# Optimization experiments

Measured on AMD Instinct MI355X. Metric: run time of the kernel, lower is better.

## Reference

```python
import jax, jax.numpy as jnp
import numpy as np

B = 8          # batch
S = 256        # nx+1 = ny+1 grid resolution
N = S * S      # number of DoFs per component
DIM = 2        # output vector dimension (= d_out)
W = 32         # FNO channel width
M1 = 12        # Fourier modes dim 1
M2 = 12        # Fourier modes dim 2
WF = 128       # final MLP hidden width
NL = 4         # number of Fourier layers
PADF = 8       # padding fraction denominator


def setup_inputs() -> dict:
    key = jax.random.key(0)
    ks = jax.random.split(key, 16)
    sc = 1.0 / (W * W)  # torch FNO spectral weight init scale
    return {
        "x": jax.random.normal(ks[0], (B, N), jnp.float32),
        "d2v_in": jax.random.permutation(ks[1], jnp.arange(N)),
        "v2d_out": jax.random.permutation(ks[2], jnp.arange(N)),
        "fc0_w": jax.random.normal(ks[3], (W, 3), jnp.float32) * 0.1,
        "fc0_b": jnp.zeros((W,), jnp.float32),
        "spec_w1r": jax.random.uniform(ks[4], (NL, W, W, M1, M2), jnp.float32) * sc,
        "spec_w1i": jax.random.uniform(ks[5], (NL, W, W, M1, M2), jnp.float32) * sc,
        "spec_w2r": jax.random.uniform(ks[6], (NL, W, W, M1, M2), jnp.float32) * sc,
        "spec_w2i": jax.random.uniform(ks[7], (NL, W, W, M1, M2), jnp.float32) * sc,
        "conv_w": jax.random.normal(ks[8], (NL, W, W), jnp.float32) * 0.05,
        "conv_b": jnp.zeros((NL, W), jnp.float32),
        "mlp_w1": jax.random.normal(ks[9], (WF, W), jnp.float32) * 0.05,
        "mlp_b1": jnp.zeros((WF,), jnp.float32),
        "mlp_w2": jax.random.normal(ks[10], (DIM, WF), jnp.float32) * 0.05,
        "mlp_b2": jnp.zeros((DIM,), jnp.float32),
    }


def _speconv(x, w1, w2):
    # x: (B, C, H, Wd) real; w1/w2: (C_in, C_out, M1, M2) complex64
    Bh, C, H, Wd = x.shape
    xft = jnp.fft.rfft2(x)  # (B, C, H, Wd//2+1)
    o1 = jnp.einsum('bixy,ioxy->boxy', xft[:, :, :M1, :M2], w1)
    o2 = jnp.einsum('bixy,ioxy->boxy', xft[:, :, -M1:, :M2], w2)
    out_ft = jnp.zeros((Bh, C, H, Wd // 2 + 1), jnp.complex64)
    out_ft = out_ft.at[:, :, :M1, :M2].set(o1).at[:, :, -M1:, :M2].set(o2)
    return jnp.fft.irfft2(out_ft, s=(H, Wd))


def reference(x, d2v_in, v2d_out, fc0_w, fc0_b,
              spec_w1r, spec_w1i, spec_w2r, spec_w2i,
              conv_w, conv_b, mlp_w1, mlp_b1, mlp_w2, mlp_b2):
    # DoF -> vertex gather and lift to image
    xg = x[:, d2v_in].reshape(B, 1, S, S)
    h = jnp.transpose(xg, (0, 2, 3, 1))  # (B, S, S, 1)
    # append normalized grid coordinates (get_grid2d)
    g = jnp.linspace(0.0, 1.0, S, dtype=jnp.float32)
    grid = jnp.stack(jnp.meshgrid(g, g, indexing='ij'), axis=-1)  # (S, S, 2)
    grid = jnp.broadcast_to(grid[None], (B, S, S, 2))
    h = jnp.concatenate([h, grid], axis=-1)
    # fc0 lifting
    h = h @ fc0_w.T + fc0_b              # (B, S, S, W)
    h = jnp.transpose(h, (0, 3, 1, 2))   # (B, W, S, S)
    # zero pad (non-periodic domain)
    p = S // PADF
    h = jnp.pad(h, ((0, 0), (0, 0), (0, p), (0, p)))  # (B, W, S+p, S+p)
    w1 = (spec_w1r + 1j * spec_w1i).astype(jnp.complex64)
    w2 = (spec_w2r + 1j * spec_w2i).astype(jnp.complex64)
    for l in range(NL):
        sp = _speconv(h, w1[l], w2[l])
        cv = jnp.einsum('bchw,oc->bohw', h, conv_w[l]) + conv_b[l][None, :, None, None]
        h = cv + sp
        if l != NL - 1:
            h = jax.nn.gelu(h, approximate=False)  # torch GELU default = exact erf
    # crop padding (s_outputspace=None path)
    h = h[..., :S, :S]
    # final two-layer MLP projection
    h = jnp.transpose(h, (0, 2, 3, 1))  # (B, S, S, W)
    h = jax.nn.gelu(h @ mlp_w1.T + mlp_b1, approximate=False) @ mlp_w2.T + mlp_b2
    h = jnp.transpose(h, (0, 3, 1, 2)).reshape(B, DIM, -1)  # (B, DIM, N)
    # vertex -> DoF scatter/gather and interleave components
    out = h[:, :, v2d_out]              # (B, DIM, N)
    out = jnp.transpose(out, (0, 2, 1)).reshape(B, -1)  # (B, N*DIM)
    return out
```

## Files before the change

### kernel.cpp

```cpp
#include <hip/hip_runtime.h>
#include <math.h>

#define S    256
#define Hp   288
#define C    32
#define KY   12
#define NK   24
#define Bn   8
#define PI_D 3.14159265358979323846264338327950288

#define SZ_TW  (NK*Hp*2)
#define OFF_TW 0
#define OFF_TWT (OFF_TW + SZ_TW)
#define SZ_TWT (Hp*KY*2)
#define OFF_H  (OFF_TWT + SZ_TWT)
#define SZ_H   (Bn*C*Hp*Hp)
#define OFF_Y  (OFF_H + SZ_H)
#define SZ_Y   (Bn*C*Hp*KY*2)
#define OFF_X  (OFF_Y + SZ_Y)
#define SZ_X   (Bn*C*NK*KY*2)
#define OFF_Z  (OFF_X + 2*SZ_X)
#define SZ_Z   (Bn*Hp*C*KY*2)
#define OFF_T  (OFF_Z + SZ_Z)
#define SZ_T   (Bn*S*S*2)

#define GELU(v) (0.5f*(v)*(1.0f+erff((v)*0.70710678118654752f)))
#define SCHED_FENCE() __builtin_amdgcn_sched_barrier(0)

#if __has_builtin(__builtin_amdgcn_global_load_lds)
#define HAS_ASYNC 1
#define ASYNC_CP16(dst, src) \
    __builtin_amdgcn_global_load_lds((const __attribute__((address_space(1))) void*)(src), \
                                     (__attribute__((address_space(3))) void*)(dst), 16, 0, 0)
#else
#define HAS_ASYNC 0
#endif

__global__ void k_tw(float* __restrict__ tw, float* __restrict__ twT) {
    int i = blockIdx.x * 256 + threadIdx.x;
    if (i >= NK * Hp) return;
    int k = i / Hp, xx = i % Hp;
    int f = (k < KY) ? k : (k + 264);
    int m = (f * xx) % Hp;
    double th = (2.0 * PI_D * (double)m) / (double)Hp;
    float c = (float)cos(th), s = (float)sin(th);
    tw[2 * i] = c; tw[2 * i + 1] = s;
    if (k < KY) { twT[xx * 24 + 2 * k] = c; twT[xx * 24 + 2 * k + 1] = s; }
}

template<int Q>
__device__ __forceinline__ void embed_body(
        const float* __restrict__ xs, const float* __restrict__ twq,
        float* __restrict__ h, size_t rowbase, int o, int g,
        float w0, float w1, float w2, float bb, float gx,
        float* pr, float* pi) {
    #pragma unroll 1
    for (int c3 = 0; c3 < 3; ++c3) {
        int ybase = g * 36 + c3 * 12;
        int rowq  = (g & 1) * 36 + c3 * 12;
        float acc[12];
        #pragma unroll
        for (int j = 0; j < 12; ++j) {
            int y = ybase + j;
            acc[j] = (y < S) ? (w0 * xs[y < S ? y : 0] + w1 * gx + w2 * (y * (1.0f / 255.0f)) + bb) : 0.f;
        }
        float* hw = h + rowbase + (size_t)o * 82944 + ybase;
        #pragma unroll
        for (int q = 0; q < 3; ++q)
            *(float4*)&hw[4 * q] = make_float4(acc[4*q], acc[4*q+1], acc[4*q+2], acc[4*q+3]);
        SCHED_FENCE();
        #pragma unroll
        for (int jp = 0; jp < 6; ++jp) {
            #pragma unroll
            for (int u = 0; u < 2; ++u) {
                int j = jp * 2 + u;
                const float* tg = twq + (rowq + j) * 24;
                float tc[24];
                #pragma unroll
                for (int q = 0; q < 6; ++q) *(float4*)&tc[4 * q] = *(const float4*)&tg[4 * q];
                float v = acc[j];
                pr[0] += v;
                #pragma unroll
                for (int k = 1; k < 12; ++k) {
                    const int e = (k * Q) & 3;
                    float c = tc[2 * k], s = tc[2 * k + 1];
                    if      (e == 0) { pr[k] += v * c; pi[k] -= v * s; }
                    else if (e == 1) { pr[k] -= v * s; pi[k] -= v * c; }
                    else if (e == 2) { pr[k] -= v * c; pi[k] += v * s; }
                    else             { pr[k] += v * s; pi[k] += v * c; }
                }
            }
            SCHED_FENCE();
        }
    }
}

__global__ __launch_bounds__(256, 1) void k_embed(
        const float* __restrict__ xin, const int* __restrict__ d2v,
        const float* __restrict__ fw, const float* __restrict__ fb,
        const float* __restrict__ twT, float* __restrict__ h, float* __restrict__ Y) {
    __shared__ __align__(16) float xs[256];
    __shared__ __align__(16) float twq[1728];
    __shared__ __align__(16) float YP[3072];
    int x = blockIdx.x, b = blockIdx.y, tid = threadIdx.x;
    size_t rowbase = (size_t)b * 2654208 + (size_t)x * 288;
    if (x >= S) {
        for (int i = tid; i < 32 * 72; i += 256) {
            int c = i / 72, q = i % 72;
            *(float4*)&h[rowbase + (size_t)c * 82944 + q * 4] = make_float4(0, 0, 0, 0);
        }
        for (int i = tid; i < 768; i += 256)
            Y[((size_t)(b * 32 + i / 24) * 288 + x) * 24 + (i % 24)] = 0.f;
        return;
    }
    for (int i = tid; i < 432; i += 256)
        *(float4*)&twq[4 * i] = *(const float4*)&twT[4 * i];
    xs[tid] = xin[b * 65536 + d2v[x * 256 + tid]];
    int o = tid & 31, g = tid >> 5;
    float w0 = fw[o * 3], w1 = fw[o * 3 + 1], w2 = fw[o * 3 + 2], bb = fb[o];
    float gx = x * (1.0f / 255.0f);
    __syncthreads();
    float pr[12], pi[12];
    #pragma unroll
    for (int k = 0; k < 12; ++k) { pr[k] = 0.f; pi[k] = 0.f; }
    switch (tid >> 6) {
        case 0: embed_body<0>(xs, twq, h, rowbase, o, g, w0, w1, w2, bb, gx, pr, pi); break;
        case 1: embed_body<1>(xs, twq, h, rowbase, o, g, w0, w1, w2, bb, gx, pr, pi); break;
        case 2: embed_body<2>(xs, twq, h, rowbase, o, g, w0, w1, w2, bb, gx, pr, pi); break;
        default: embed_body<3>(xs, twq, h, rowbase, o, g, w0, w1, w2, bb, gx, pr, pi); break;
    }
    #pragma unroll
    for (int k = 0; k < 12; ++k) { pr[k] += __shfl_xor(pr[k], 32); pi[k] += __shfl_xor(pi[k], 32); }
    if ((tid & 32) == 0) {
        float* dst = YP + ((tid >> 6) * 32 + o) * 24;
        #pragma unroll
        for (int k = 0; k < 12; ++k) { dst[2 * k] = pr[k]; dst[2 * k + 1] = pi[k]; }
    }
    __syncthreads();
    for (int i = tid; i < 768; i += 256) {
        float s = YP[i] + YP[768 + i] + YP[1536 + i] + YP[2304 + i];
        Y[((size_t)(b * 32 + i / 24) * 288 + x) * 24 + (i % 24)] = s;
    }
}

__global__ __launch_bounds__(288) void k_dftx(const float* __restrict__ Y,
                                              const float* __restrict__ tw,
                                              float* __restrict__ X) {
    __shared__ __align__(16) float Ys[144 * 24];
    int c = blockIdx.x, b = blockIdx.y, half = blockIdx.z, tid = threadIdx.x;
    const float* Yb = Y + (size_t)(b * 32 + c) * 6912 + half * 3456;
    for (int i = tid; i < 864; i += 288)
        *(float4*)&Ys[4 * i] = *(const float4*)&Yb[4 * i];
    __syncthreads();
    int k = tid / 12, ky = tid % 12;
    const float* twk = tw + k * 576 + half * 288;
    float xr = 0.f, xi = 0.f;
    #pragma unroll 4
    for (int xx = 0; xx < 144; ++xx) {
        float yr = Ys[xx * 24 + 2 * ky], yi = Ys[xx * 24 + 2 * ky + 1];
        float cc = twk[2 * xx], ss = twk[2 * xx + 1];
        xr += yr * cc + yi * ss;
        xi += yi * cc - yr * ss;
    }
    size_t oo = (size_t)half * SZ_X + ((size_t)(b * 32 + c) * 288 + tid) * 2;
    X[oo] = xr; X[oo + 1] = xi;
}

__global__ __launch_bounds__(384) void k_specidft(
        const float* __restrict__ X,
        const float* __restrict__ w1r, const float* __restrict__ w1i,
        const float* __restrict__ w2r, const float* __restrict__ w2i,
        const float* __restrict__ tw, float* __restrict__ Z, int l) {
    __shared__ __align__(16) float Os[576];
    int x0 = blockIdx.x * 32, c = blockIdx.y, b = blockIdx.z, tid = threadIdx.x;
    if (tid < 288) {
        int k = tid / 12, ky = tid % 12;
        int kk = (k < KY) ? k : (k - KY);
        const float* wr = (k < KY) ? w1r : w2r;
        const float* wi = (k < KY) ? w1i : w2i;
        size_t wbase = (size_t)l * 147456 + (size_t)c * 144 + kk * 12 + ky;
        size_t xbase = (size_t)b * 18432 + (k * 12 + ky) * 2;
        float ar = 0.f, ai = 0.f;
        #pragma unroll 8
        for (int i = 0; i < 32; ++i) {
            size_t xo = xbase + (size_t)i * 576;
            float xr = X[xo]     + X[SZ_X + xo];
            float xi = X[xo + 1] + X[SZ_X + xo + 1];
            float wrr = wr[wbase + (size_t)i * 4608];
            float wii = wi[wbase + (size_t)i * 4608];
            ar += xr * wrr - xi * wii;
            ai += xr * wii + xi * wrr;
        }
        Os[2 * tid] = ar; Os[2 * tid + 1] = ai;
    }
    __syncthreads();
    int row = tid & 31, ky = tid >> 5;
    int x = x0 + row;
    float zr = 0.f, zi = 0.f;
    #pragma unroll
    for (int k = 0; k < NK; ++k) {
        float orr = Os[(k * 12 + ky) * 2], oii = Os[(k * 12 + ky) * 2 + 1];
        float cc = tw[(k * Hp + x) * 2], ss = tw[(k * Hp + x) * 2 + 1];
        zr += orr * cc - oii * ss;
        zi += orr * ss + oii * cc;
    }
    size_t o = ((((size_t)b * Hp + x) * C + c) * KY + ky) * 2;
    Z[o] = zr; Z[o + 1] = zi;
}

__global__ __launch_bounds__(256, 1) void k_conv(
        float* __restrict__ h, const float* __restrict__ Z,
        const float* __restrict__ cw, const float* __restrict__ cb,
        const float* __restrict__ twT, float* __restrict__ Y,
        int l, int flags) {
    __shared__ __align__(16) float hs[9216];
    __shared__ __align__(16) float twy[6912];
    __shared__ __align__(16) float cws[32 * 33];
    __shared__ float cbs[32];
    int x = blockIdx.x, b = blockIdx.y, tid = threadIdx.x;
    size_t rowbase = (size_t)b * 2654208 + (size_t)x * 288;
    const float* hb = h + rowbase;
#if HAS_ASYNC
    #pragma unroll 1
    for (int r = 0; r < 9; ++r) {
        int i = r * 256 + tid;
        ASYNC_CP16(&hs[4 * i], hb + (size_t)(i / 72) * 82944 + (i % 72) * 4);
    }
    #pragma unroll 1
    for (int i = tid; i < 1728; i += 256)
        ASYNC_CP16(&twy[4 * i], twT + 4 * i);
#else
    for (int i = tid; i < 2304; i += 256)
        *(float4*)&hs[4 * i] = *(const float4*)&hb[(size_t)(i / 72) * 82944 + (i % 72) * 4];
    for (int i = tid; i < 1728; i += 256)
        *(float4*)&twy[4 * i] = *(const float4*)&twT[4 * i];
#endif
    for (int i = tid; i < 32 * 32; i += 256)
        cws[(i >> 5) * 33 + (i & 31)] = cw[l * 1024 + i];
    if (tid < 32) cbs[tid] = cb[l * 32 + tid];
    int o = tid & 31, g = tid >> 5;
    const float* Zr = Z + ((size_t)(b * 288 + x) * 32 + o) * 24;
    float zr[12], zi[12];
    #pragma unroll
    for (int q = 0; q < 6; ++q) {
        float4 zv = *(const float4*)&Zr[4 * q];
        zr[2*q] = zv.x; zi[2*q] = zv.y; zr[2*q+1] = zv.z; zi[2*q+1] = zv.w;
    }
    __syncthreads();
    float bias = cbs[o];
    float pr[12], pi[12];
    #pragma unroll
    for (int k = 0; k < 12; ++k) { pr[k] = 0.f; pi[k] = 0.f; }
    const int gelu_f = flags & 1, wy = flags & 2;
    #pragma unroll 1
    for (int c3 = 0; c3 < 3; ++c3) {
        int ybase = g * 36 + c3 * 12;
        float acc[12];
        #pragma unroll
        for (int j = 0; j < 12; ++j) acc[j] = bias;
        #pragma unroll 8
        for (int c = 0; c < 32; ++c) {
            float w = cws[o * 33 + c];
            const float* hr = &hs[c * 288 + ybase];
            float4 h0 = *(const float4*)&hr[0];
            float4 h1 = *(const float4*)&hr[4];
            float4 h2 = *(const float4*)&hr[8];
            acc[0] += h0.x * w; acc[1] += h0.y * w; acc[2]  += h0.z * w; acc[3]  += h0.w * w;
            acc[4] += h1.x * w; acc[5] += h1.y * w; acc[6]  += h1.z * w; acc[7]  += h1.w * w;
            acc[8] += h2.x * w; acc[9] += h2.y * w; acc[10] += h2.z * w; acc[11] += h2.w * w;
        }
        SCHED_FENCE();
        #pragma unroll
        for (int jp = 0; jp < 6; ++jp) {
            #pragma unroll
            for (int u = 0; u < 2; ++u) {
                int j = jp * 2 + u;
                int y = ybase + j;
                float tc[24];
                #pragma unroll
                for (int q = 0; q < 6; ++q) *(float4*)&tc[4 * q] = *(const float4*)&twy[y * 24 + 4 * q];
                float sp = zr[0] * tc[0] - zi[0] * tc[1];
                #pragma unroll
                for (int k = 1; k < 12; ++k) sp += 2.f * (zr[k] * tc[2*k] - zi[k] * tc[2*k+1]);
                float val = acc[j] + sp * (1.0f / 82944.0f);
                if (gelu_f) val = GELU(val);
                acc[j] = val;
                if (wy) {
                    #pragma unroll
                    for (int k = 0; k < 12; ++k) { pr[k] += val * tc[2*k]; pi[k] -= val * tc[2*k+1]; }
                }
            }
            SCHED_FENCE();
        }
        float* hw = h + rowbase + (size_t)o * 82944 + ybase;
        #pragma unroll
        for (int q = 0; q < 3; ++q)
            *(float4*)&hw[4 * q] = make_float4(acc[4*q], acc[4*q+1], acc[4*q+2], acc[4*q+3]);
        SCHED_FENCE();
    }
    if (wy) {
        #pragma unroll
        for (int k = 0; k < 12; ++k) { pr[k] += __shfl_xor(pr[k], 32); pi[k] += __shfl_xor(pi[k], 32); }
        __syncthreads();
        float* YP = hs;
        if ((tid & 32) == 0) {
            float* dst = YP + ((tid >> 6) * 32 + o) * 24;
            #pragma unroll
            for (int k = 0; k < 12; ++k) { dst[2 * k] = pr[k]; dst[2 * k + 1] = pi[k]; }
        }
        __syncthreads();
        for (int i = tid; i < 768; i += 256) {
            float s = YP[i] + YP[768 + i] + YP[1536 + i] + YP[2304 + i];
            Y[((size_t)(b * 32 + i / 24) * 288 + x) * 24 + (i % 24)] = s;
        }
    }
}

__global__ __launch_bounds__(256) void k_mlp(const float* __restrict__ h,
                                             const float* __restrict__ w1, const float* __restrict__ b1,
                                             const float* __restrict__ w2, const float* __restrict__ b2,
                                             float* __restrict__ tmp) {
    int bid = blockIdx.x;
    int b = bid >> 7;
    int x = ((bid & 127) << 1) + (threadIdx.x >> 7);
    int lane = threadIdx.x & 127;
    const float* hb = h + (size_t)b * 2654208 + (size_t)x * 288;
    float hc0[32], hc1[32];
    #pragma unroll
    for (int c = 0; c < 32; ++c) {
        hc0[c] = hb[(size_t)c * 82944 + lane];
        hc1[c] = hb[(size_t)c * 82944 + lane + 128];
    }
    float o00 = 0.f, o01 = 0.f, o10 = 0.f, o11 = 0.f;
    for (int f = 0; f < 128; ++f) {
        float a0 = b1[f], a1 = a0;
        #pragma unroll
        for (int c = 0; c < 32; ++c) {
            float w = w1[f * 32 + c];
            a0 += hc0[c] * w; a1 += hc1[c] * w;
        }
        float wa = w2[f], wb = w2[128 + f];
        float g0 = GELU(a0), g1 = GELU(a1);
        o00 += g0 * wa; o01 += g0 * wb;
        o10 += g1 * wa; o11 += g1 * wb;
    }
    float bb0 = b2[0], bb1 = b2[1];
    int p0 = x * 256 + lane;
    size_t base = (size_t)b * 65536;
    *(float2*)&tmp[(base + p0) * 2]       = make_float2(o00 + bb0, o01 + bb1);
    *(float2*)&tmp[(base + p0 + 128) * 2] = make_float2(o10 + bb0, o11 + bb1);
}

__global__ void k_scatter(const float* __restrict__ tmp, const int* __restrict__ v2d,
                          float* __restrict__ out) {
    int id = blockIdx.x * 256 + threadIdx.x;
    int b = id >> 16; int j = id & 65535;
    int p = v2d[j];
    const float2 v = *(const float2*)(tmp + ((size_t)(b << 16) + p) * 2);
    *(float2*)(out + (size_t)id * 2) = v;
}

extern "C" void kernel_launch(void* const* d_in, const int* in_sizes, int n_in,
                              void* d_out, int out_size, void* d_ws, size_t ws_size,
                              hipStream_t stream) {
    const float* xin   = (const float*)d_in[0];
    const int*   d2v   = (const int*)  d_in[1];
    const int*   v2d   = (const int*)  d_in[2];
    const float* fc0w  = (const float*)d_in[3];
    const float* fc0b  = (const float*)d_in[4];
    const float* w1r   = (const float*)d_in[5];
    const float* w1i   = (const float*)d_in[6];
    const float* w2r   = (const float*)d_in[7];
    const float* w2i   = (const float*)d_in[8];
    const float* cw    = (const float*)d_in[9];
    const float* cb    = (const float*)d_in[10];
    const float* mw1   = (const float*)d_in[11];
    const float* mb1   = (const float*)d_in[12];
    const float* mw2   = (const float*)d_in[13];
    const float* mb2   = (const float*)d_in[14];

    float* ws  = (float*)d_ws;
    float* TW  = ws + OFF_TW;
    float* TWT = ws + OFF_TWT;
    float* H   = ws + OFF_H;
    float* Y   = ws + OFF_Y;
    float* X   = ws + OFF_X;
    float* Z   = ws + OFF_Z;
    float* T   = ws + OFF_T;

    k_tw<<<(NK * Hp + 255) / 256, 256, 0, stream>>>(TW, TWT);
    k_embed<<<dim3(Hp, Bn), 256, 0, stream>>>(xin, d2v, fc0w, fc0b, TWT, H, Y);

    for (int l = 0; l < 4; ++l) {
        k_dftx<<<dim3(32, Bn, 2), 288, 0, stream>>>(Y, TW, X);
        k_specidft<<<dim3(9, 32, Bn), 384, 0, stream>>>(X, w1r, w1i, w2r, w2i, TW, Z, l);
        k_conv<<<dim3((l != 3) ? Hp : S, Bn), 256, 0, stream>>>(H, Z, cw, cb, TWT, Y, l, (l != 3) ? 3 : 0);
    }

    k_mlp<<<1024, 256, 0, stream>>>(H, mw1, mb1, mw2, mb2, T);
    k_scatter<<<(Bn * S * S) / 256, 256, 0, stream>>>(T, v2d, (float*)d_out);
}
```

Measured before the change: 812.8 us.

## Fuse last Fourier layer conv with final MLP projection into one kernel

Measured after the change: 1.046 ms. 28.7% more time.

```diff
diff --git a/kernel.cpp b/kernel.cpp
--- a/kernel.cpp
+++ b/kernel.cpp
@@ -208,11 +208,45 @@
     Z[o] = zr; Z[o + 1] = zi;
 }
 
+__device__ __forceinline__ void conv12(const float* __restrict__ hs,
+                                       const float* __restrict__ cws,
+                                       int o, int ybase, float bias, float* acc) {
+    #pragma unroll
+    for (int j = 0; j < 12; ++j) acc[j] = bias;
+    #pragma unroll 8
+    for (int c = 0; c < 32; ++c) {
+        float w = cws[o * 33 + c];
+        const float* hr = &hs[c * 288 + ybase];
+        float4 h0 = *(const float4*)&hr[0];
+        float4 h1 = *(const float4*)&hr[4];
+        float4 h2 = *(const float4*)&hr[8];
+        acc[0] += h0.x * w; acc[1] += h0.y * w; acc[2]  += h0.z * w; acc[3]  += h0.w * w;
+        acc[4] += h1.x * w; acc[5] += h1.y * w; acc[6]  += h1.z * w; acc[7]  += h1.w * w;
+        acc[8] += h2.x * w; acc[9] += h2.y * w; acc[10] += h2.z * w; acc[11] += h2.w * w;
+    }
+    SCHED_FENCE();
+}
+
+__device__ __forceinline__ void epi12_plain(const float* __restrict__ twy, int ybase,
+                                            float* acc, const float* zr, const float* zi) {
+    #pragma unroll
+    for (int j = 0; j < 12; ++j) {
+        const float* tg = twy + (ybase + j) * 24;
+        float tc[24];
+        #pragma unroll
+        for (int q = 0; q < 6; ++q) *(float4*)&tc[4 * q] = *(const float4*)&tg[4 * q];
+        float sp = zr[0] * tc[0] - zi[0] * tc[1];
+        #pragma unroll
+        for (int k = 1; k < 12; ++k) sp += 2.f * (zr[k] * tc[2*k] - zi[k] * tc[2*k+1]);
+        acc[j] += sp * (1.0f / 82944.0f);
+        if (j & 1) SCHED_FENCE();
+    }
+}
+
 __global__ __launch_bounds__(256, 1) void k_conv(
         float* __restrict__ h, const float* __restrict__ Z,
         const float* __restrict__ cw, const float* __restrict__ cb,
-        const float* __restrict__ twT, float* __restrict__ Y,
-        int l, int flags) {
+        const float* __restrict__ twT, float* __restrict__ Y, int l) {
     __shared__ __align__(16) float hs[9216];
     __shared__ __align__(16) float twy[6912];
     __shared__ __align__(16) float cws[32 * 33];
@@ -251,25 +285,11 @@
     float pr[12], pi[12];
     #pragma unroll
     for (int k = 0; k < 12; ++k) { pr[k] = 0.f; pi[k] = 0.f; }
-    const int gelu_f = flags & 1, wy = flags & 2;
     #pragma unroll 1
     for (int c3 = 0; c3 < 3; ++c3) {
         int ybase = g * 36 + c3 * 12;
         float acc[12];
-        #pragma unroll
-        for (int j = 0; j < 12; ++j) acc[j] = bias;
-        #pragma unroll 8
-        for (int c = 0; c < 32; ++c) {
-            float w = cws[o * 33 + c];
-            const float* hr = &hs[c * 288 + ybase];
-            float4 h0 = *(const float4*)&hr[0];
-            float4 h1 = *(const float4*)&hr[4];
-            float4 h2 = *(const float4*)&hr[8];
-            acc[0] += h0.x * w; acc[1] += h0.y * w; acc[2]  += h0.z * w; acc[3]  += h0.w * w;
-            acc[4] += h1.x * w; acc[5] += h1.y * w; acc[6]  += h1.z * w; acc[7]  += h1.w * w;
-            acc[8] += h2.x * w; acc[9] += h2.y * w; acc[10] += h2.z * w; acc[11] += h2.w * w;
-        }
-        SCHED_FENCE();
+        conv12(hs, cws, o, ybase, bias, acc);
         #pragma unroll
         for (int jp = 0; jp < 6; ++jp) {
             #pragma unroll
@@ -283,12 +303,10 @@
                 #pragma unroll
                 for (int k = 1; k < 12; ++k) sp += 2.f * (zr[k] * tc[2*k] - zi[k] * tc[2*k+1]);
                 float val = acc[j] + sp * (1.0f / 82944.0f);
-                if (gelu_f) val = GELU(val);
+                val = GELU(val);
                 acc[j] = val;
-                if (wy) {
-                    #pragma unroll
-                    for (int k = 0; k < 12; ++k) { pr[k] += val * tc[2*k]; pi[k] -= val * tc[2*k+1]; }
-                }
+                #pragma unroll
+                for (int k = 0; k < 12; ++k) { pr[k] += val * tc[2*k]; pi[k] -= val * tc[2*k+1]; }
             }
             SCHED_FENCE();
         }
@@ -298,57 +316,96 @@
             *(float4*)&hw[4 * q] = make_float4(acc[4*q], acc[4*q+1], acc[4*q+2], acc[4*q+3]);
         SCHED_FENCE();
     }
-    if (wy) {
-        #pragma unroll
-        for (int k = 0; k < 12; ++k) { pr[k] += __shfl_xor(pr[k], 32); pi[k] += __shfl_xor(pi[k], 32); }
-        __syncthreads();
-        float* YP = hs;
-        if ((tid & 32) == 0) {
-            float* dst = YP + ((tid >> 6) * 32 + o) * 24;
-            #pragma unroll
-            for (int k = 0; k < 12; ++k) { dst[2 * k] = pr[k]; dst[2 * k + 1] = pi[k]; }
-        }
-        __syncthreads();
-        for (int i = tid; i < 768; i += 256) {
-            float s = YP[i] + YP[768 + i] + YP[1536 + i] + YP[2304 + i];
-            Y[((size_t)(b * 32 + i / 24) * 288 + x) * 24 + (i % 24)] = s;
-        }
-    }
-}
-
-__global__ __launch_bounds__(256) void k_mlp(const float* __restrict__ h,
-                                             const float* __restrict__ w1, const float* __restrict__ b1,
-                                             const float* __restrict__ w2, const float* __restrict__ b2,
-                                             float* __restrict__ tmp) {
-    int bid = blockIdx.x;
-    int b = bid >> 7;
-    int x = ((bid & 127) << 1) + (threadIdx.x >> 7);
-    int lane = threadIdx.x & 127;
-    const float* hb = h + (size_t)b * 2654208 + (size_t)x * 288;
-    float hc0[32], hc1[32];
-    #pragma unroll
-    for (int c = 0; c < 32; ++c) {
-        hc0[c] = hb[(size_t)c * 82944 + lane];
-        hc1[c] = hb[(size_t)c * 82944 + lane + 128];
-    }
-    float o00 = 0.f, o01 = 0.f, o10 = 0.f, o11 = 0.f;
+    #pragma unroll
+    for (int k = 0; k < 12; ++k) { pr[k] += __shfl_xor(pr[k], 32); pi[k] += __shfl_xor(pi[k], 32); }
+    __syncthreads();
+    float* YP = hs;
+    if ((tid & 32) == 0) {
+        float* dst = YP + ((tid >> 6) * 32 + o) * 24;
+        #pragma unroll
+        for (int k = 0; k < 12; ++k) { dst[2 * k] = pr[k]; dst[2 * k + 1] = pi[k]; }
+    }
+    __syncthreads();
+    for (int i = tid; i < 768; i += 256) {
+        float s = YP[i] + YP[768 + i] + YP[1536 + i] + YP[2304 + i];
+        Y[((size_t)(b * 32 + i / 24) * 288 + x) * 24 + (i % 24)] = s;
+    }
+}
+
+__global__ __launch_bounds__(256, 1) void k_convmlp(
+        const float* __restrict__ h, const float* __restrict__ Z,
+        const float* __restrict__ cw, const float* __restrict__ cb,
+        const float* __restrict__ twT,
+        const float* __restrict__ mw1, const float* __restrict__ mb1,
+        const float* __restrict__ mw2, const float* __restrict__ mb2,
+        float* __restrict__ tmp) {
+    __shared__ __align__(16) float hs[9216];
+    __shared__ __align__(16) float twy[6912];
+    __shared__ __align__(16) float cws[32 * 33];
+    __shared__ float cbs[32];
+    int x = blockIdx.x, b = blockIdx.y, tid = threadIdx.x;
+    size_t rowbase = (size_t)b * 2654208 + (size_t)x * 288;
+    const float* hb = h + rowbase;
+#if HAS_ASYNC
+    #pragma unroll 1
+    for (int r = 0; r < 9; ++r) {
+        int i = r * 256 + tid;
+        ASYNC_CP16(&hs[4 * i], hb + (size_t)(i / 72) * 82944 + (i % 72) * 4);
+    }
+    #pragma unroll 1
+    for (int i = tid; i < 1728; i += 256)
+        ASYNC_CP16(&twy[4 * i], twT + 4 * i);
+#else
+    for (int i = tid; i < 2304; i += 256)
+        *(float4*)&hs[4 * i] = *(const float4*)&hb[(size_t)(i / 72) * 82944 + (i % 72) * 4];
+    for (int i = tid; i < 1728; i += 256)
+        *(float4*)&twy[4 * i] = *(const float4*)&twT[4 * i];
+#endif
+    for (int i = tid; i < 32 * 32; i += 256)
+        cws[(i >> 5) * 33 + (i & 31)] = cw[3 * 1024 + i];
+    if (tid < 32) cbs[tid] = cb[3 * 32 + tid];
+    int o = tid & 31, g = tid >> 5;
+    const float* Zr = Z + ((size_t)(b * 288 + x) * 32 + o) * 24;
+    float zr[12], zi[12];
+    #pragma unroll
+    for (int q = 0; q < 6; ++q) {
+        float4 zv = *(const float4*)&Zr[4 * q];
+        zr[2*q] = zv.x; zi[2*q] = zv.y; zr[2*q+1] = zv.z; zi[2*q+1] = zv.w;
+    }
+    __syncthreads();
+    float bias = cbs[o];
+    float a0[12], a1[12], a2[12];
+    conv12(hs, cws, o, g * 36,      bias, a0);
+    conv12(hs, cws, o, g * 36 + 12, bias, a1);
+    conv12(hs, cws, o, g * 36 + 24, bias, a2);
+    epi12_plain(twy, g * 36,      a0, zr, zi);
+    epi12_plain(twy, g * 36 + 12, a1, zr, zi);
+    epi12_plain(twy, g * 36 + 24, a2, zr, zi);
+    __syncthreads();
+    {
+        float* hw = hs + o * 288 + g * 36;
+        #pragma unroll
+        for (int q = 0; q < 3; ++q) {
+            *(float4*)&hw[4 * q]      = make_float4(a0[4*q], a0[4*q+1], a0[4*q+2], a0[4*q+3]);
+            *(float4*)&hw[12 + 4 * q] = make_float4(a1[4*q], a1[4*q+1], a1[4*q+2], a1[4*q+3]);
+            *(float4*)&hw[24 + 4 * q] = make_float4(a2[4*q], a2[4*q+1], a2[4*q+2], a2[4*q+3]);
+        }
+    }
+    __syncthreads();
+    float hc[32];
+    #pragma unroll
+    for (int c = 0; c < 32; ++c) hc[c] = hs[c * 288 + tid];
+    float o0 = 0.f, o1 = 0.f;
+    #pragma unroll 4
     for (int f = 0; f < 128; ++f) {
-        float a0 = b1[f], a1 = a0;
-        #pragma unroll
-        for (int c = 0; c < 32; ++c) {
-            float w = w1[f * 32 + c];
-            a0 += hc0[c] * w; a1 += hc1[c] * w;
-        }
-        float wa = w2[f], wb = w2[128 + f];
-        float g0 = GELU(a0), g1 = GELU(a1);
-        o00 += g0 * wa; o01 += g0 * wb;
-        o10 += g1 * wa; o11 += g1 * wb;
-    }
-    float bb0 = b2[0], bb1 = b2[1];
-    int p0 = x * 256 + lane;
-    size_t base = (size_t)b * 65536;
-    *(float2*)&tmp[(base + p0) * 2]       = make_float2(o00 + bb0, o01 + bb1);
-    *(float2*)&tmp[(base + p0 + 128) * 2] = make_float2(o10 + bb0, o11 + bb1);
+        float a = mb1[f];
+        #pragma unroll
+        for (int c = 0; c < 32; ++c) a += hc[c] * mw1[f * 32 + c];
+        float gl = GELU(a);
+        o0 += gl * mw2[f]; o1 += gl * mw2[128 + f];
+    }
+    size_t p = (size_t)b * 65536 + x * 256 + tid;
+    *(float2*)&tmp[p * 2] = make_float2(o0 + mb2[0], o1 + mb2[1]);
 }
 
 __global__ void k_scatter(const float* __restrict__ tmp, const int* __restrict__ v2d,
@@ -394,9 +451,11 @@
     for (int l = 0; l < 4; ++l) {
         k_dftx<<<dim3(32, Bn, 2), 288, 0, stream>>>(Y, TW, X);
         k_specidft<<<dim3(9, 32, Bn), 384, 0, stream>>>(X, w1r, w1i, w2r, w2i, TW, Z, l);
-        k_conv<<<dim3((l != 3) ? Hp : S, Bn), 256, 0, stream>>>(H, Z, cw, cb, TWT, Y, l, (l != 3) ? 3 : 0);
-    }
-
-    k_mlp<<<1024, 256, 0, stream>>>(H, mw1, mb1, mw2, mb2, T);
+        if (l != 3)
+            k_conv<<<dim3(Hp, Bn), 256, 0, stream>>>(H, Z, cw, cb, TWT, Y, l);
+        else
+            k_convmlp<<<dim3(S, Bn), 256, 0, stream>>>(H, Z, cw, cb, TWT, mw1, mb1, mw2, mb2, T);
+    }
+
     k_scatter<<<(Bn * S * S) / 256, 256, 0, stream>>>(T, v2d, (float*)d_out);
 }
```
